# Optimization experiments

Hardware: AMD Instinct MI355X
Metric: run time of the kernel (lower is better)

The kernel has to match this reference:

```python
import jax, jax.numpy as jnp
import numpy as np

B, S, D, H = 8, 1024, 1024, 16
HD = D // H  # 64


def setup_inputs() -> dict:
    key = jax.random.key(0)
    ks = jax.random.split(key, 10)
    s = 1.0 / np.sqrt(HD)
    x = jax.random.normal(ks[0], (B, S, D), dtype=jnp.float32)
    mask = jax.random.randint(ks[1], (B, S), 0, 2).astype(bool)  # True = padded
    # per-head q/k/v projections of SimpleAttention, stacked over heads
    Wq = jax.random.normal(ks[2], (H, HD, HD), dtype=jnp.float32) * s
    bq = jnp.zeros((H, HD), dtype=jnp.float32)
    Wk = jax.random.normal(ks[3], (H, HD, HD), dtype=jnp.float32) * s
    bk = jnp.zeros((H, HD), dtype=jnp.float32)
    Wv = jax.random.normal(ks[4], (H, HD, HD), dtype=jnp.float32) * s
    bv = jnp.zeros((H, HD), dtype=jnp.float32)
    # out_proj: Linear(dim, dim)
    Wo = jax.random.normal(ks[5], (D, D), dtype=jnp.float32) * (1.0 / np.sqrt(D))
    bo = jnp.zeros((D,), dtype=jnp.float32)
    return {"x": x, "mask": mask, "Wq": Wq, "bq": bq, "Wk": Wk, "bk": bk,
            "Wv": Wv, "bv": bv, "Wo": Wo, "bo": bo}


def reference(x, mask, Wq, bq, Wk, bk, Wv, bv, Wo, bo):
    b, s, d = x.shape
    xh = x.reshape(b, s, H, HD).transpose(0, 2, 1, 3)  # (b, h, s, hd)
    # per-head linear projections (batched over heads via einsum)
    q = jnp.einsum('bhsd,hde->bhse', xh, Wq) + bq[None, :, None, :]
    k = jnp.einsum('bhsd,hde->bhse', xh, Wk) + bk[None, :, None, :]
    v = jnp.einsum('bhsd,hde->bhse', xh, Wv) + bv[None, :, None, :]
    scale = 1.0 / jnp.sqrt(jnp.asarray(HD, dtype=x.dtype))
    scores = jnp.einsum('bhqd,bhkd->bhqk', q, k) * scale  # (b, h, s, s)
    # key-padding mask: True = padded -> -inf on key axis
    neg = jnp.asarray(jnp.finfo(x.dtype).min, dtype=x.dtype)
    scores = jnp.where(mask[:, None, None, :], neg, scores)
    attn = jax.nn.softmax(scores, axis=-1)
    out = jnp.einsum('bhqk,bhkd->bhqd', attn, v)  # (b, h, s, hd)
    concat = out.transpose(0, 2, 1, 3).reshape(b, s, d)
    # out_proj (dropout is identity in eval)
    return concat @ Wo.T + bo
```

## Files before the change

### kernel.cpp

```cpp
#include <hip/hip_runtime.h>
#include <float.h>

#define B_ 8
#define S_ 1024
#define D_ 1024
#define H_ 16
#define HD_ 64

typedef __attribute__((ext_vector_type(8))) _Float16 half8;
typedef __attribute__((ext_vector_type(4))) _Float16 half4;
typedef __attribute__((ext_vector_type(4))) float f32x4;

__device__ __forceinline__ void gld16(const void* g, void* l) {
  __builtin_amdgcn_global_load_lds(
      (const __attribute__((address_space(1))) void*)g,
      (__attribute__((address_space(3))) void*)l, 16, 0, 0);
}

__global__ void detect_mask_kernel(const unsigned int* __restrict__ m, int* __restrict__ flag) {
  __shared__ int bad;
  if (threadIdx.x == 0) bad = 0;
  __syncthreads();
  int my = 0;
  for (int i = threadIdx.x; i < 2048; i += 256) {
    if (m[i] & ~1u) my = 1;
  }
  if (my) atomicOr(&bad, 1);
  __syncthreads();
  if (threadIdx.x == 0) *flag = bad;
}

__global__ void expand_mask_kernel(const unsigned char* __restrict__ mb,
                                   const int* __restrict__ mi,
                                   const int* __restrict__ flag,
                                   float* __restrict__ maskadd) {
  int i = blockIdx.x * 256 + threadIdx.x;
  if (i < B_ * S_) {
    int f = *flag;
    int v = f ? (int)mb[i] : mi[i];
    maskadd[i] = (v != 0) ? -FLT_MAX : 0.0f;
  }
}

__global__ void cast_wo_kernel(const float* __restrict__ Wo, _Float16* __restrict__ Wo16) {
  int i = blockIdx.x * 256 + threadIdx.x;
  if (i < D_ * D_) Wo16[i] = (_Float16)Wo[i];
}

__global__ void cast_wqkv_kernel(const float* __restrict__ Wq, const float* __restrict__ bq,
                                 const float* __restrict__ Wk, const float* __restrict__ bk,
                                 const float* __restrict__ Wv, const float* __restrict__ bv,
                                 _Float16* __restrict__ Wc, float* __restrict__ bs) {
  int idx = blockIdx.x * 256 + threadIdx.x;
  if (idx < 16 * 3 * 64 * 64) {
    int d = idx & 63;
    int e = (idx >> 6) & 63;
    int t2 = idx >> 12;
    int m = t2 % 3, h = t2 / 3;
    int src = h * 4096 + d * 64 + e;
    float v = (m == 0) ? Wq[src] * 0.18033688f : (m == 1) ? Wk[src] : Wv[src];
    Wc[idx] = (_Float16)v;
  }
  if (idx < 3072) {
    int m = idx >> 10, he = idx & 1023;
    float v = (m == 0) ? bq[he] * 0.18033688f : (m == 1) ? bk[he] : bv[he];
    bs[idx] = v;
  }
}

__global__ __launch_bounds__(256) void qkv_kernel(
    const float* __restrict__ x, const _Float16* __restrict__ Wc,
    const float* __restrict__ bs,
    _Float16* __restrict__ q16, _Float16* __restrict__ k16, _Float16* __restrict__ vT16) {
  const int tile = blockIdx.x & 15;
  const int bh = blockIdx.x >> 4;
  const int b = bh >> 4, h = bh & 15;
  const int s0 = tile * 64;
  const int w = threadIdx.x >> 6, lane = threadIdx.x & 63;
  const int col = lane & 15, quad = lane >> 4;
  const int srow = s0 + w * 16 + col;

  const float* xr = x + ((size_t)(b * S_) + srow) * D_ + h * HD_;
  f32x4 x0a = *(const f32x4*)(xr + quad * 8);
  f32x4 x0b = *(const f32x4*)(xr + quad * 8 + 4);
  f32x4 x1a = *(const f32x4*)(xr + 32 + quad * 8);
  f32x4 x1b = *(const f32x4*)(xr + 32 + quad * 8 + 4);
  half8 Xf0, Xf1;
#pragma unroll
  for (int j = 0; j < 4; ++j) {
    Xf0[j] = (_Float16)x0a[j];
    Xf0[4 + j] = (_Float16)x0b[j];
    Xf1[j] = (_Float16)x1a[j];
    Xf1[4 + j] = (_Float16)x1b[j];
  }

  const _Float16* wbase = Wc + (size_t)h * 3 * 4096;
  const f32x4 z4 = {0.f, 0.f, 0.f, 0.f};
#pragma unroll
  for (int mm = 0; mm < 2; ++mm) {
    _Float16* outp = mm ? k16 : q16;
    const _Float16* wm = wbase + mm * 4096;
#pragma unroll
    for (int et = 0; et < 4; ++et) {
      const _Float16* wr = wm + (et * 16 + col) * 64;
      half8 W0 = *(const half8*)(wr + quad * 8);
      half8 W1 = *(const half8*)(wr + 32 + quad * 8);
      f32x4 c = __builtin_amdgcn_mfma_f32_16x16x32_f16(W0, Xf0, z4, 0, 0, 0);
      c = __builtin_amdgcn_mfma_f32_16x16x32_f16(W1, Xf1, c, 0, 0, 0);
      f32x4 bb = *(const f32x4*)(bs + mm * 1024 + h * 64 + et * 16 + quad * 4);
      half4 o;
#pragma unroll
      for (int r = 0; r < 4; ++r) o[r] = (_Float16)(c[r] + bb[r]);
      *(half4*)(outp + ((size_t)bh * S_ + srow) * HD_ + et * 16 + quad * 4) = o;
    }
  }
  {
    const _Float16* wm = wbase + 2 * 4096;
#pragma unroll
    for (int et = 0; et < 4; ++et) {
      const _Float16* wr = wm + (et * 16 + col) * 64;
      half8 W0 = *(const half8*)(wr + quad * 8);
      half8 W1 = *(const half8*)(wr + 32 + quad * 8);
      f32x4 c = __builtin_amdgcn_mfma_f32_16x16x32_f16(Xf0, W0, z4, 0, 0, 0);
      c = __builtin_amdgcn_mfma_f32_16x16x32_f16(Xf1, W1, c, 0, 0, 0);
      float bb = bs[2048 + h * 64 + et * 16 + col];
      half4 o;
#pragma unroll
      for (int r = 0; r < 4; ++r) o[r] = (_Float16)(c[r] + bb);
      *(half4*)(vT16 + ((size_t)bh * HD_ + et * 16 + col) * S_ + s0 + w * 16 + quad * 4) = o;
    }
  }
}

__global__ __launch_bounds__(256, 4) void attn_kernel(
    const _Float16* __restrict__ q, const _Float16* __restrict__ k,
    const _Float16* __restrict__ vT, const float* __restrict__ maskadd,
    _Float16* __restrict__ att) {
  __shared__ alignas(16) _Float16 Ks[2][64 * 64];
  __shared__ alignas(16) _Float16 Vs[2][64 * 64];
  const int bh = blockIdx.x & 127;
  const int qblk = blockIdx.x >> 7;
  const int b = bh >> 4, h = bh & 15;
  const int wv = threadIdx.x >> 6;
  const int lane = threadIdx.x & 63;
  const int quad = lane >> 4, col = lane & 15;
  const int c7 = col & 7;
  const int q0 = qblk * 128 + wv * 32;

  const _Float16* __restrict__ kb = k + (size_t)bh * S_ * HD_;
  const _Float16* __restrict__ vb = vT + (size_t)bh * HD_ * S_;
  const float* __restrict__ mrow = maskadd + b * S_;

  const int jj0 = wv * 128 + lane, jj1 = jj0 + 64;
  const int r0s = jj0 >> 3, r1s = jj1 >> 3;
  const int sg0 = (jj0 & 7) ^ (r0s & 7), sg1 = (jj1 & 7) ^ (r1s & 7);
  const int offK0 = r0s * 128 + sg0 * 16, offK1 = r1s * 128 + sg1 * 16;
  const int offV0 = r0s * 2048 + sg0 * 16, offV1 = r1s * 2048 + sg1 * 16;
  const int ldsb0 = wv * 1024, ldsb1 = wv * 1024 + 512;

  half8 Qf[2][2];
#pragma unroll
  for (int qt = 0; qt < 2; ++qt) {
    const _Float16* qrow = q + ((size_t)bh * S_ + q0 + qt * 16 + col) * HD_;
    Qf[qt][0] = *(const half8*)(qrow + quad * 8);
    Qf[qt][1] = *(const half8*)(qrow + 32 + quad * 8);
  }

  const f32x4 z4 = {0.f, 0.f, 0.f, 0.f};
  f32x4 O[2][4];
#pragma unroll
  for (int qt = 0; qt < 2; ++qt)
#pragma unroll
    for (int et = 0; et < 4; ++et) O[qt][et] = z4;
  float l[2] = {0.f, 0.f};

  {
    const char* kg = (const char*)kb;
    const char* vg = (const char*)vb;
    gld16(kg + offK0, &Ks[0][ldsb0]);
    gld16(kg + offK1, &Ks[0][ldsb1]);
    gld16(vg + offV0, &Vs[0][ldsb0]);
    gld16(vg + offV1, &Vs[0][ldsb1]);
  }
  int cur = 0;
  for (int c = 0; c < 16; ++c) {
    __syncthreads();
    if (c < 15) {
      const char* kg = (const char*)kb + (size_t)(c + 1) * 8192;
      const char* vg = (const char*)vb + (size_t)(c + 1) * 128;
      gld16(kg + offK0, &Ks[cur ^ 1][ldsb0]);
      gld16(kg + offK1, &Ks[cur ^ 1][ldsb1]);
      gld16(vg + offV0, &Vs[cur ^ 1][ldsb0]);
      gld16(vg + offV1, &Vs[cur ^ 1][ldsb1]);
    }
    const int kk0 = c * 64;
    const _Float16* Kb_ = &Ks[cur][0];
    const _Float16* Vb_ = &Vs[cur][0];
    f32x4 mkv[4];
#pragma unroll
    for (int kt = 0; kt < 4; ++kt) mkv[kt] = *(const f32x4*)(mrow + kk0 + kt * 16 + quad * 4);
    half8 Kf[4][2];
#pragma unroll
    for (int kt = 0; kt < 4; ++kt) {
      const int rb = (kt * 16 + col) * 64;
      Kf[kt][0] = *(const half8*)&Kb_[rb + ((quad) ^ c7) * 8];
      Kf[kt][1] = *(const half8*)&Kb_[rb + ((4 + quad) ^ c7) * 8];
    }
    f32x4 st[2][4];
#pragma unroll
    for (int qt = 0; qt < 2; ++qt)
#pragma unroll
      for (int kt = 0; kt < 4; ++kt) {
        f32x4 s = __builtin_amdgcn_mfma_f32_16x16x32_f16(Kf[kt][0], Qf[qt][0], mkv[kt], 0, 0, 0);
        st[qt][kt] = __builtin_amdgcn_mfma_f32_16x16x32_f16(Kf[kt][1], Qf[qt][1], s, 0, 0, 0);
      }
    half4 Vf[4][4];
#pragma unroll
    for (int kt = 0; kt < 4; ++kt) {
      const int sb = ((kt * 2 + (quad >> 1)) ^ c7) * 8 + (quad & 1) * 4;
#pragma unroll
      for (int et = 0; et < 4; ++et) Vf[kt][et] = *(const half4*)&Vb_[(et * 16 + col) * 64 + sb];
    }
#pragma unroll
    for (int qt = 0; qt < 2; ++qt) {
      float p[16];
#pragma unroll
      for (int kt = 0; kt < 4; ++kt)
#pragma unroll
        for (int r = 0; r < 4; ++r) p[kt * 4 + r] = __builtin_amdgcn_exp2f(st[qt][kt][r]);
      float s01 = (p[0] + p[1]) + (p[2] + p[3]);
      float s23 = (p[4] + p[5]) + (p[6] + p[7]);
      float s45 = (p[8] + p[9]) + (p[10] + p[11]);
      float s67 = (p[12] + p[13]) + (p[14] + p[15]);
      l[qt] += (s01 + s23) + (s45 + s67);
      half4 ph[4];
#pragma unroll
      for (int kt = 0; kt < 4; ++kt)
#pragma unroll
        for (int r = 0; r < 4; ++r) ph[kt][r] = (_Float16)p[kt * 4 + r];
#pragma unroll
      for (int et = 0; et < 4; ++et) {
        f32x4 o = O[qt][et];
#pragma unroll
        for (int kt = 0; kt < 4; ++kt)
          o = __builtin_amdgcn_mfma_f32_16x16x16f16(Vf[kt][et], ph[kt], o, 0, 0, 0);
        O[qt][et] = o;
      }
    }
    cur ^= 1;
  }
#pragma unroll
  for (int qt = 0; qt < 2; ++qt) {
    float lt = l[qt];
    lt += __shfl_xor(lt, 16);
    lt += __shfl_xor(lt, 32);
    const float inv = 1.0f / lt;
    _Float16* orow = att + ((size_t)(b * S_ + q0 + qt * 16 + col)) * D_ + h * HD_;
#pragma unroll
    for (int et = 0; et < 4; ++et) {
      half4 o;
#pragma unroll
      for (int r = 0; r < 4; ++r) o[r] = (_Float16)(O[qt][et][r] * inv);
      *(half4*)(orow + et * 16 + quad * 4) = o;
    }
  }
}

__global__ __launch_bounds__(256, 4) void outproj_kernel(
    const _Float16* __restrict__ A, const _Float16* __restrict__ Bw,
    const float* __restrict__ bo, float* __restrict__ C) {
  __shared__ _Float16 As[128 * 40];
  __shared__ _Float16 Bs[128 * 40];
  const int m0 = (int)(blockIdx.x >> 3) * 128;
  const int n0 = (int)(blockIdx.x & 7) * 128;
  const int t = threadIdx.x;
  const int lane = t & 63, wv = t >> 6;
  const int quad = lane >> 4, col = lane & 15;
  const int mw = (wv >> 1) * 64, nw = (wv & 1) * 64;
  const int row = t >> 1, seg = t & 1;
  f32x4 acc[16];
  const f32x4 z4 = {0.f, 0.f, 0.f, 0.f};
#pragma unroll
  for (int i = 0; i < 16; ++i) acc[i] = z4;
  for (int kt = 0; kt < D_; kt += 32) {
    __syncthreads();
    {
      const _Float16* ga = A + (size_t)(m0 + row) * D_ + kt + seg * 16;
      *(half8*)&As[row * 40 + seg * 16] = *(const half8*)ga;
      *(half8*)&As[row * 40 + seg * 16 + 8] = *(const half8*)(ga + 8);
      const _Float16* gb = Bw + (size_t)(n0 + row) * D_ + kt + seg * 16;
      *(half8*)&Bs[row * 40 + seg * 16] = *(const half8*)gb;
      *(half8*)&Bs[row * 40 + seg * 16 + 8] = *(const half8*)(gb + 8);
    }
    __syncthreads();
    half8 aF[4], bF[4];
#pragma unroll
    for (int mt = 0; mt < 4; ++mt) aF[mt] = *(const half8*)&As[(mw + mt * 16 + col) * 40 + quad * 8];
#pragma unroll
    for (int nt = 0; nt < 4; ++nt) bF[nt] = *(const half8*)&Bs[(nw + nt * 16 + col) * 40 + quad * 8];
#pragma unroll
    for (int mt = 0; mt < 4; ++mt)
#pragma unroll
      for (int nt = 0; nt < 4; ++nt)
        acc[mt * 4 + nt] =
            __builtin_amdgcn_mfma_f32_16x16x32_f16(aF[mt], bF[nt], acc[mt * 4 + nt], 0, 0, 0);
  }
#pragma unroll
  for (int mt = 0; mt < 4; ++mt)
#pragma unroll
    for (int nt = 0; nt < 4; ++nt) {
      f32x4 a = acc[mt * 4 + nt];
      const int n = n0 + nw + nt * 16 + col;
      const float bb = bo[n];
#pragma unroll
      for (int r = 0; r < 4; ++r) {
        const int mrow = m0 + mw + mt * 16 + quad * 4 + r;
        C[(size_t)mrow * D_ + n] = a[r] + bb;
      }
    }
}

extern "C" void kernel_launch(void* const* d_in, const int* in_sizes, int n_in,
                              void* d_out, int out_size, void* d_ws, size_t ws_size,
                              hipStream_t stream) {
  const float* x  = (const float*)d_in[0];
  const float* Wq = (const float*)d_in[2];
  const float* bq = (const float*)d_in[3];
  const float* Wk = (const float*)d_in[4];
  const float* bk = (const float*)d_in[5];
  const float* Wv = (const float*)d_in[6];
  const float* bv = (const float*)d_in[7];
  const float* Wo = (const float*)d_in[8];
  const float* bo = (const float*)d_in[9];

  float* wsf     = (float*)d_ws;
  float* maskadd = wsf;
  int*   flag    = (int*)(wsf + 8192);
  const size_t NE = (size_t)B_ * H_ * S_ * HD_;
  _Float16* hws  = (_Float16*)(wsf + 16384);
  _Float16* q16  = hws;
  _Float16* k16  = q16 + NE;
  _Float16* vT16 = k16 + NE;
  _Float16* att16 = vT16 + NE;
  _Float16* Wo16 = att16 + NE;
  _Float16* Wc   = Wo16 + 1048576;
  float*    bs   = (float*)(Wc + 196608);

  detect_mask_kernel<<<1, 256, 0, stream>>>((const unsigned int*)d_in[1], flag);
  expand_mask_kernel<<<(B_ * S_ + 255) / 256, 256, 0, stream>>>(
      (const unsigned char*)d_in[1], (const int*)d_in[1], flag, maskadd);
  cast_wo_kernel<<<(D_ * D_ + 255) / 256, 256, 0, stream>>>(Wo, Wo16);
  cast_wqkv_kernel<<<(16 * 3 * 64 * 64 + 255) / 256, 256, 0, stream>>>(
      Wq, bq, Wk, bk, Wv, bv, Wc, bs);
  qkv_kernel<<<B_ * H_ * (S_ / 64), 256, 0, stream>>>(x, Wc, bs, q16, k16, vT16);
  attn_kernel<<<B_ * H_ * (S_ / 128), 256, 0, stream>>>(q16, k16, vT16, maskadd, att16);
  outproj_kernel<<<(B_ * S_ / 128) * (D_ / 128), 256, 0, stream>>>(att16, Wo16, bo, (float*)d_out);
}
```

Measured before the change: 212.9 us.

## Use direct global-to-LDS loads with XOR swizzle and K=64 tiles in outproj GEMM

The output-projection GEMM now stages A and B tiles with global_load_lds DMA instead of loading into registers and then storing to LDS. The K tile doubles to 64, which halves the number of barrier pairs. An XOR swizzle on 16-byte segments replaces the padded layout to avoid LDS bank conflicts. LDS use per block grows, which may lower occupancy, and loads are still not double-buffered.

```diff
diff --git a/kernel.cpp b/kernel.cpp
--- a/kernel.cpp
+++ b/kernel.cpp
@@ -269,41 +269,57 @@
 __global__ __launch_bounds__(256, 4) void outproj_kernel(
     const _Float16* __restrict__ A, const _Float16* __restrict__ Bw,
     const float* __restrict__ bo, float* __restrict__ C) {
-  __shared__ _Float16 As[128 * 40];
-  __shared__ _Float16 Bs[128 * 40];
+  __shared__ alignas(16) _Float16 As[128 * 64];
+  __shared__ alignas(16) _Float16 Bs[128 * 64];
   const int m0 = (int)(blockIdx.x >> 3) * 128;
   const int n0 = (int)(blockIdx.x & 7) * 128;
   const int t = threadIdx.x;
   const int lane = t & 63, wv = t >> 6;
   const int quad = lane >> 4, col = lane & 15;
   const int mw = (wv >> 1) * 64, nw = (wv & 1) * 64;
-  const int row = t >> 1, seg = t & 1;
+
+  int rowS[4], segS[4];
+#pragma unroll
+  for (int sweep = 0; sweep < 4; ++sweep) {
+    const int s = sweep * 256 + wv * 64 + lane;
+    rowS[sweep] = s >> 3;
+    segS[sweep] = (s & 7) ^ (rowS[sweep] & 7);
+  }
+
   f32x4 acc[16];
   const f32x4 z4 = {0.f, 0.f, 0.f, 0.f};
 #pragma unroll
   for (int i = 0; i < 16; ++i) acc[i] = z4;
-  for (int kt = 0; kt < D_; kt += 32) {
+
+  for (int kt = 0; kt < 16; ++kt) {
+#pragma unroll
+    for (int sweep = 0; sweep < 4; ++sweep) {
+      const int ldsbase = (sweep * 256 + wv * 64) * 8;
+      gld16(A + (size_t)(m0 + rowS[sweep]) * D_ + kt * 64 + segS[sweep] * 8, &As[ldsbase]);
+      gld16(Bw + (size_t)(n0 + rowS[sweep]) * D_ + kt * 64 + segS[sweep] * 8, &Bs[ldsbase]);
+    }
     __syncthreads();
-    {
-      const _Float16* ga = A + (size_t)(m0 + row) * D_ + kt + seg * 16;
-      *(half8*)&As[row * 40 + seg * 16] = *(const half8*)ga;
-      *(half8*)&As[row * 40 + seg * 16 + 8] = *(const half8*)(ga + 8);
-      const _Float16* gb = Bw + (size_t)(n0 + row) * D_ + kt + seg * 16;
-      *(half8*)&Bs[row * 40 + seg * 16] = *(const half8*)gb;
-      *(half8*)&Bs[row * 40 + seg * 16 + 8] = *(const half8*)(gb + 8);
+#pragma unroll
+    for (int ks = 0; ks < 2; ++ks) {
+      half8 aF[4], bF[4];
+#pragma unroll
+      for (int mt = 0; mt < 4; ++mt) {
+        const int row = mw + mt * 16 + col;
+        aF[mt] = *(const half8*)&As[row * 64 + (((ks * 4 + quad) ^ (row & 7)) * 8)];
+      }
+#pragma unroll
+      for (int nt = 0; nt < 4; ++nt) {
+        const int row = nw + nt * 16 + col;
+        bF[nt] = *(const half8*)&Bs[row * 64 + (((ks * 4 + quad) ^ (row & 7)) * 8)];
+      }
+#pragma unroll
+      for (int mt = 0; mt < 4; ++mt)
+#pragma unroll
+        for (int nt = 0; nt < 4; ++nt)
+          acc[mt * 4 + nt] =
+              __builtin_amdgcn_mfma_f32_16x16x32_f16(aF[mt], bF[nt], acc[mt * 4 + nt], 0, 0, 0);
     }
     __syncthreads();
-    half8 aF[4], bF[4];
-#pragma unroll
-    for (int mt = 0; mt < 4; ++mt) aF[mt] = *(const half8*)&As[(mw + mt * 16 + col) * 40 + quad * 8];
-#pragma unroll
-    for (int nt = 0; nt < 4; ++nt) bF[nt] = *(const half8*)&Bs[(nw + nt * 16 + col) * 40 + quad * 8];
-#pragma unroll
-    for (int mt = 0; mt < 4; ++mt)
-#pragma unroll
-      for (int nt = 0; nt < 4; ++nt)
-        acc[mt * 4 + nt] =
-            __builtin_amdgcn_mfma_f32_16x16x32_f16(aF[mt], bF[nt], acc[mt * 4 + nt], 0, 0, 0);
   }
 #pragma unroll
   for (int mt = 0; mt < 4; ++mt)
```

Measured after the change: 209.1 us. No clear change (-1.7%).
